# Performance work log

Measured on AMD Instinct MI355X. Metric: run time of the kernel, lower is better.

Reference implementation:

```python
import jax, jax.numpy as jnp
import numpy as np
import math

B, T, D, S, V = 128, 32, 64, 32, 8192
MAX_REC = 8
PONDER = 0.01
TWO_PI = 2.0 * math.pi


def setup_inputs():
    key = jax.random.key(0)
    ks = jax.random.split(key, 12)
    sd = 1.0 / math.sqrt(D)
    g = lambda k, shape, s: jax.random.normal(k, shape, jnp.float32) * s
    return {
        "x_seq": jax.random.randint(ks[0], (B, T), 0, V),
        "encoder_emb": g(ks[1], (V, 2 * D), 0.02),
        "vq_emb": g(ks[2], (V, 2 * D), sd),
        "norm_rg": jnp.ones((D,), jnp.float32), "norm_rb": jnp.zeros((D,), jnp.float32),
        "norm_ig": jnp.ones((D,), jnp.float32), "norm_ib": jnp.zeros((D,), jnp.float32),
        "qkv_Wr": g(ks[3], (3, D, D), sd), "qkv_br": g(ks[4], (3, D), sd),
        "qkv_Wi": g(ks[5], (3, D, D), sd), "qkv_bi": g(ks[6], (3, D), sd),
        "gate_w": g(ks[7], (2 * D,), sd), "gate_b": jnp.zeros((), jnp.float32),
        "arb_W": g(ks[8], (3, 2 * D), sd), "arb_b": jnp.zeros((3,), jnp.float32),
        "dec_W": g(ks[9], (V, 2 * D), sd), "dec_b": jnp.zeros((V,), jnp.float32),
        "halt_bias": jnp.asarray(3.0, jnp.float32),
        "input_gate": jnp.asarray(0.0, jnp.float32),
    }


def _ln(x, g, b, eps=1e-5):
    mu = x.mean(-1, keepdims=True)
    var = ((x - mu) ** 2).mean(-1, keepdims=True)
    return (x - mu) * jax.lax.rsqrt(var + eps) * g + b


def _forward(x_seq, encoder_emb, vq_emb, norm_rg, norm_rb, norm_ig, norm_ib,
             qkv_Wr, qkv_br, qkv_Wi, qkv_bi, gate_w, gate_b, arb_W, arb_b,
             dec_W, dec_b, halt_bias, input_gate):
    sg = jax.lax.stop_gradient
    e_sq = (vq_emb ** 2).sum(-1)  # [V]
    alpha = jax.nn.sigmoid(input_gate)
    bias = jax.nn.softplus(halt_bias)

    def clin(xr, xi, Wr, br, Wi, bi):
        # torch ComplexLinear: real = fc_r(xr) - fc_i(xi); imag = fc_r(xi) + fc_i(xr)
        return (xr @ Wr.T + br) - (xi @ Wi.T + bi), (xi @ Wr.T + br) + (xr @ Wi.T + bi)

    def mem_write(gr, gi, mr, mi):
        flat = jnp.concatenate([gr, gi], -1)
        wg = jax.nn.sigmoid(flat @ gate_w + gate_b)[:, None, None]  # [B,1,1]
        shr, shi = jnp.roll(mr, 1, axis=1), jnp.roll(mi, 1, axis=1)
        hr = wg * gr[:, None, :] + (1.0 - wg) * shr[:, :1]
        hi = wg * gi[:, None, :] + (1.0 - wg) * shi[:, :1]
        return jnp.concatenate([hr, shr[:, 1:]], 1), jnp.concatenate([hi, shi[:, 1:]], 1)

    def time_step(carry, xt):
        gw_r, gw_i, mem_r, mem_i = carry
        x_r, x_i = xt
        gw_r = alpha * gw_r + (1.0 - alpha) * x_r
        gw_i = alpha * gw_i + (1.0 - alpha) * x_i
        active = jnp.ones((B,), jnp.float32)
        acc_vq = jnp.zeros((B,), jnp.float32)
        acc_ent = jnp.zeros((B,), jnp.float32)
        acc_pond = jnp.zeros((B,), jnp.float32)
        acc_ph = jnp.zeros((B,), jnp.float32)
        fin_idx = jnp.zeros((B,), jnp.int32)
        prev_ang = jnp.arctan2(gw_i, gw_r)
        for _ in range(MAX_REC):
            cr = _ln(gw_r, norm_rg, norm_rb)
            ci = _ln(gw_i, norm_ig, norm_ib)
            z_flat = jnp.concatenate([cr, ci], -1)  # [B,2D]
            # squared-euclidean scores; argmin identical to cdist argmin
            d2 = (z_flat ** 2).sum(-1, keepdims=True) - 2.0 * (z_flat @ vq_emb.T) + e_sq
            idx = jnp.argmin(d2, -1).astype(jnp.int32)
            z_q = vq_emb[idx]
            vq_loss = ((z_q - sg(z_flat)) ** 2).mean(-1) + 0.25 * ((sg(z_q) - z_flat) ** 2).mean(-1)
            z_st = z_flat + sg(z_q - z_flat)  # straight-through
            counts = jnp.zeros((V,), jnp.float32).at[idx].add(1.0) / B
            entropy = -(counts * jnp.log(counts + 1e-10)).sum()
            v_r, v_i = z_st[:, :D], z_st[:, D:]
            # Hermitian gating
            qr, qi = clin(cr, ci, qkv_Wr[0], qkv_br[0], qkv_Wi[0], qkv_bi[0])
            kr, ki = clin(cr, ci, qkv_Wr[1], qkv_br[1], qkv_Wi[1], qkv_bi[1])
            vr2, vi2 = clin(cr, ci, qkv_Wr[2], qkv_br[2], qkv_Wi[2], qkv_bi[2])
            gate = jax.nn.sigmoid((qr * kr + qi * ki).sum(-1, keepdims=True))
            g_r, g_i = vr2 * gate, vi2 * gate
            # memory read (Re<m, q> attention over slots)
            sim = jnp.einsum('bsd,bd->bs', mem_r, cr) + jnp.einsum('bsd,bd->bs', mem_i, ci)
            attn = jax.nn.softmax(sim, -1)
            m_r = jnp.einsum('bs,bsd->bd', attn, mem_r)
            m_i = jnp.einsum('bs,bsd->bd', attn, mem_i)
            gates = jax.nn.softmax(z_flat @ arb_W.T + arb_b, -1)  # [B,3]
            upd_r = gates[:, 0:1] * g_r + gates[:, 1:2] * m_r + gates[:, 2:3] * v_r
            upd_i = gates[:, 0:1] * g_i + gates[:, 1:2] * m_i + gates[:, 2:3] * v_i
            cand_r = 0.6 * cr + 0.4 * upd_r
            cand_i = 0.6 * ci + 0.4 * upd_i
            ang = jnp.arctan2(cand_i, cand_r)
            diff = jnp.abs(ang - prev_ang)
            diff = jnp.minimum(diff, TWO_PI - diff)
            acc_ph = acc_ph + active * diff.mean(-1)
            prev_ang = ang
            halt_prob = jax.nn.sigmoid(bias - vq_loss)
            should_stop = (halt_prob > 0.5).astype(jnp.float32)
            acc_pond = acc_pond + active * PONDER
            mflat = active > 0.5
            acc_vq = jnp.where(mflat, vq_loss, acc_vq)
            acc_ent = jnp.where(mflat, entropy, acc_ent)
            fin_idx = jnp.where(mflat, idx, fin_idx)
            am = mflat[:, None]
            gw_r = jnp.where(am, cand_r, gw_r)
            gw_i = jnp.where(am, cand_i, gw_i)
            active = active * (1.0 - should_stop)
        mem_r, mem_i = mem_write(gw_r, gw_i, mem_r, mem_i)
        stats_t = jnp.stack([acc_vq.mean(), acc_ent.mean(), acc_pond.mean(), acc_ph.mean()])
        return (gw_r, gw_i, mem_r, mem_i), (gw_r, gw_i, fin_idx, stats_t)

    emb = encoder_emb[x_seq]  # [B,T,2D]
    xr = jnp.transpose(emb[..., :D], (1, 0, 2))  # [T,B,D]
    xi = jnp.transpose(emb[..., D:], (1, 0, 2))
    init = (jnp.zeros((B, D), jnp.float32), jnp.zeros((B, D), jnp.float32),
            jnp.zeros((B, S, D), jnp.float32), jnp.zeros((B, S, D), jnp.float32))
    _, (out_r, out_i, idxs, stats) = jax.lax.scan(time_step, init, (xr, xi))
    out = jnp.concatenate([jnp.transpose(out_r, (1, 0, 2)),
                           jnp.transpose(out_i, (1, 0, 2))], -1)  # [B,T,2D]
    logits = out @ dec_W.T + dec_b  # [B,T,V]
    return logits, stats.sum(0) / T, jnp.transpose(idxs)  # [B,T]


def reference(x_seq, encoder_emb, vq_emb, norm_rg, norm_rb, norm_ig, norm_ib, qkv_Wr, qkv_br, qkv_Wi, qkv_bi, gate_w, gate_b, arb_W, arb_b, dec_W, dec_b, halt_bias, input_gate):
    return _forward(x_seq, encoder_emb, vq_emb, norm_rg, norm_rb, norm_ig, norm_ib,
                    qkv_Wr, qkv_br, qkv_Wi, qkv_bi, gate_w, gate_b, arb_W, arb_b,
                    dec_W, dec_b, halt_bias, input_gate)
```

## Files before the change

kernel.cpp:

```cpp
#include <hip/hip_runtime.h>
#include <math.h>

#define TT 32
#define MAXREC 8
#define NBLK 256
#define NTHR 512

#define OFF_ZBUF   0u
#define OFF_ZBUFB  65536u
#define OFF_KEYS   98304u
#define OFF_ZDONE  229376u
#define OFF_ESQ    231424u
#define OFF_RST    264192u
#define OFF_OUTHB  266240u
#define OFF_WB     1314816u

#define SENT 0x7FFFFFFFu
#define IDXM 0x1FFFu
#define LOGN 33554432u
#define TWO_PI_F 6.283185307179586f

typedef float f32x4 __attribute__((ext_vector_type(4)));
typedef short bf16x8 __attribute__((ext_vector_type(8)));
typedef unsigned long long u64;

__device__ __forceinline__ float wredsum(float v) {
#pragma unroll
  for (int m = 32; m > 0; m >>= 1) v += __shfl_xor(v, m);
  return v;
}
__device__ __forceinline__ u64 shflx64(u64 v, int m) {
  int lo = __shfl_xor((int)(unsigned)(v & 0xffffffffull), m);
  int hi = __shfl_xor((int)(unsigned)(v >> 32), m);
  return ((u64)(unsigned)hi << 32) | (unsigned)lo;
}
__device__ __forceinline__ u64 packkey(float d, unsigned c) {
  unsigned u = __float_as_uint(d);
  u = (u & 0x80000000u) ? ~u : (u | 0x80000000u);
  return ((u64)u << 32) | c;
}
__device__ __forceinline__ float unpackd2(u64 key) {
  unsigned hi = (unsigned)(key >> 32);
  unsigned orig = (hi & 0x80000000u) ? (hi & 0x7fffffffu) : ~hi;
  return __uint_as_float(orig);
}
__device__ __forceinline__ unsigned short f2bf(float f) {
  unsigned u = __float_as_uint(f);
  unsigned r = (u >> 16) & 1u;
  u += 0x7fffu + r;
  return (unsigned short)(u >> 16);
}

__device__ __forceinline__ u64 ld_coh64(const u64* p) {
  u64 v;
  asm volatile("global_load_dwordx2 %0, %1, off sc0 sc1\n\ts_waitcnt vmcnt(0)"
               : "=&v"(v) : "v"(p) : "memory");
  return v;
}
__device__ __forceinline__ void st_coh_f32(float* p, float v) {
  asm volatile("global_store_dword %0, %1, off sc0 sc1" :: "v"(p), "v"(v) : "memory");
}
__device__ __forceinline__ void st_coh32(unsigned* p, unsigned v) {
  asm volatile("global_store_dword %0, %1, off sc0 sc1" :: "v"(p), "v"(v) : "memory");
}
__device__ __forceinline__ void st_coh64(u64* p, u64 v) {
  asm volatile("global_store_dwordx2 %0, %1, off sc0 sc1" :: "v"(p), "v"(v) : "memory");
}
__device__ __forceinline__ void drain_vm() {
  asm volatile("s_waitcnt vmcnt(0)" ::: "memory");
}
__device__ __forceinline__ void ld4w(const float* base,
    unsigned o0, unsigned o1, unsigned o2, unsigned o3,
    f32x4& a0, f32x4& a1, f32x4& a2, f32x4& a3) {
  asm volatile(
      "global_load_dwordx4 %0, %4, %8 sc0 sc1\n\t"
      "global_load_dwordx4 %1, %5, %8 sc0 sc1\n\t"
      "global_load_dwordx4 %2, %6, %8 sc0 sc1\n\t"
      "global_load_dwordx4 %3, %7, %8 sc0 sc1\n\t"
      "s_waitcnt vmcnt(0)"
      : "=&v"(a0), "=&v"(a1), "=&v"(a2), "=&v"(a3)
      : "v"(o0), "v"(o1), "v"(o2), "v"(o3), "s"(base)
      : "memory");
}

__global__ __launch_bounds__(512) void sacrsn_init(char* __restrict__ ws) {
  u64* zd = (u64*)(ws + OFF_ZDONE);
  u64* fin = (u64*)(ws + OFF_KEYS);
  (void)fin;
  if (threadIdx.x < 256) ((u64*)zd)[threadIdx.x] = 0ull;
}

__global__ __launch_bounds__(256) void k_prepv(const float* __restrict__ vqe,
                                               char* __restrict__ ws) {
  unsigned short* vqeB = (unsigned short*)(ws + OFF_WB);
  float* esqG = (float*)(ws + OFF_ESQ);
  const int i = (blockIdx.x * 256 + threadIdx.x) * 4;
  float4 v = *(const float4*)(vqe + i);
  ushort4 o;
  o.x = f2bf(v.x); o.y = f2bf(v.y); o.z = f2bf(v.z); o.w = f2bf(v.w);
  *(ushort4*)(vqeB + i) = o;
  if (blockIdx.x < 32) {
    const int c = blockIdx.x * 256 + threadIdx.x;
    const float4* e = (const float4*)(vqe + ((size_t)c << 7));
    float s = 0.f;
#pragma unroll 8
    for (int k4 = 0; k4 < 32; ++k4) {
      float4 q = e[k4];
      s = fmaf(q.x, q.x, fmaf(q.y, q.y, fmaf(q.z, q.z, fmaf(q.w, q.w, s))));
    }
    esqG[c] = s;
  }
}

__global__ __launch_bounds__(256) void k_prepd(const float* __restrict__ dW,
                                               char* __restrict__ ws) {
  unsigned short* dWb = (unsigned short*)(ws + OFF_WB);
  const int i = (blockIdx.x * 256 + threadIdx.x) * 4;
  float4 v = *(const float4*)(dW + i);
  ushort4 o;
  o.x = f2bf(v.x); o.y = f2bf(v.y); o.z = f2bf(v.z); o.w = f2bf(v.w);
  *(ushort4*)(dWb + i) = o;
}

__global__ __launch_bounds__(NTHR) void sacrsn_main(
    const int* __restrict__ x_seq, const float* __restrict__ enc,
    const float* __restrict__ vqe,
    const float* __restrict__ nrg, const float* __restrict__ nrb,
    const float* __restrict__ nig, const float* __restrict__ nib,
    const float* __restrict__ qWr, const float* __restrict__ qbr,
    const float* __restrict__ qWi, const float* __restrict__ qbi,
    const float* __restrict__ gtw, const float* __restrict__ gtb,
    const float* __restrict__ aW, const float* __restrict__ ab,
    const float* __restrict__ hbp, const float* __restrict__ igp,
    float* __restrict__ dout, char* __restrict__ ws)
{
  float* zbuf = (float*)(ws + OFF_ZBUF);
  unsigned* zbufB32 = (unsigned*)(ws + OFF_ZBUFB);
  u64*   keys = (u64*)(ws + OFF_KEYS);
  u64*   zdone64 = (u64*)(ws + OFF_ZDONE);
  const float* esqG = (const float*)(ws + OFF_ESQ);
  const unsigned short* vqeB = (const unsigned short*)(ws + OFF_WB);
  u64*   finalA = (u64*)(ws + OFF_KEYS);
  unsigned short* outhB = (unsigned short*)(ws + OFF_OUTHB);
  float* rst  = (float*)(ws + OFF_RST);
  finalA = (u64*)(ws + OFF_ZDONE + 1024u);
  finalA = (u64*)(ws + OFF_ZDONE + 8u);

  const int tid = threadIdx.x;
  const int wv = tid >> 6, ln = tid & 63;
  const int blk = blockIdx.x;
  const bool owner = (blk < 128);

  __shared__ float memLr[32 * 65];
  __shared__ float memLi[32 * 65];
  __shared__ float gwrowL[128], pangL[64], zfmL[128], zqL[128];
  __shared__ float qkL[6][64], simL[32], attnL[32], mrL[64], miL[64];
  __shared__ unsigned idxL[128] __attribute__((aligned(16)));
  __shared__ u64 key128L[128], kred[128];
  __shared__ float arbWL[3 * 128];
  __shared__ float scalL[8], entpL[2], vqpL[2], wsumL[2], z2pL[2];
  __shared__ float accL[4], totL[4];
  __shared__ float dmeanS;
  __shared__ u64 actM[2], actN[2];
  __shared__ unsigned pollOK, pollSent, mfS;
  __shared__ float z2L[128], sz2L[128];
  __shared__ u64 rowminU[128];
  __shared__ unsigned candL[8192];
  __shared__ unsigned candCount;

  const float alpha = 1.0f / (1.0f + expf(-igp[0]));
  const float onema = 1.0f - alpha;
  const float hbias = log1pf(expf(hbp[0]));
  const float gtb0 = gtb[0];

  if (!owner) {
    const int s = blk - 128;
    const int w = tid >> 6, l = tid & 63;
    const int ar = l & 15, kg = l >> 4;
    unsigned k = 0;
    while (true) {
      bool done = false;
      while (true) {
        if (tid == 0) { pollOK = 1u; pollSent = 1u; }
        __syncthreads();
        if (tid < 128) {
          u64 v = ld_coh64(&zdone64[tid * 2]);
          unsigned lo = (unsigned)v;
          if ((int)(lo - (k + 1u)) < 0) pollOK = 0u;
          if (lo != SENT) pollSent = 0u;
          if (lo == k + 1u) z2L[tid] = __uint_as_float((unsigned)(v >> 32));
        }
        __syncthreads();
        if (pollSent) { done = true; break; }
        if (pollOK) break;
        __builtin_amdgcn_s_sleep(1);
      }
      if (done) break;
      if (tid < 128) { sz2L[tid] = sqrtf(z2L[tid]); rowminU[tid] = ~0ull; }
      if (tid == 0) candCount = 0u;
      __syncthreads();
      f32x4 af0, af1, af2, af3;
      {
        const unsigned rb = (unsigned)((w * 16 + ar) * 256 + kg * 16);
        ld4w((const float*)(ws + OFF_ZBUFB), rb, rb + 64u, rb + 128u, rb + 192u,
             af0, af1, af2, af3);
      }
      bf16x8 afr[4];
      afr[0] = *(bf16x8*)&af0; afr[1] = *(bf16x8*)&af1;
      afr[2] = *(bf16x8*)&af2; afr[3] = *(bf16x8*)&af3;
      f32x4 dc[4];
#pragma unroll
      for (int nt = 0; nt < 4; ++nt) dc[nt] = (f32x4){0.f, 0.f, 0.f, 0.f};
#pragma unroll
      for (int kc = 0; kc < 4; ++kc) {
#pragma unroll
        for (int nt = 0; nt < 4; ++nt) {
          bf16x8 b = *(const bf16x8*)(vqeB + (((size_t)(s * 64 + nt * 16 + ar)) << 7)
                                      + kc * 32 + kg * 8);
          dc[nt] = __builtin_amdgcn_mfma_f32_16x16x32_bf16(afr[kc], b, dc[nt], 0, 0, 0);
        }
      }
      float aV[4][4], eV[4][4], Lmin[4];
#pragma unroll
      for (int rr = 0; rr < 4; ++rr) Lmin[rr] = 1e30f;
#pragma unroll
      for (int nt = 0; nt < 4; ++nt) {
        const int code = s * 64 + nt * 16 + ar;
        const float es = esqG[code];
        const float se = sqrtf(es);
#pragma unroll
        for (int rr = 0; rr < 4; ++rr) {
          const int row = w * 16 + kg * 4 + rr;
          float av = (z2L[row] - 2.0f * dc[nt][rr]) + es;
          float ev = fmaf(0.0082f * sz2L[row], se, 1e-3f);
          aV[nt][rr] = av; eV[nt][rr] = ev;
          float ae = av + ev;
          if (ae < Lmin[rr]) Lmin[rr] = ae;
        }
      }
#pragma unroll
      for (int m2 = 1; m2 < 16; m2 <<= 1)
#pragma unroll
        for (int rr = 0; rr < 4; ++rr) {
          float o = __shfl_xor(Lmin[rr], m2);
          if (o < Lmin[rr]) Lmin[rr] = o;
        }
#pragma unroll
      for (int nt = 0; nt < 4; ++nt)
#pragma unroll
        for (int rr = 0; rr < 4; ++rr)
          if (aV[nt][rr] - eV[nt][rr] <= Lmin[rr]) {
            const unsigned row = (unsigned)(w * 16 + kg * 4 + rr);
            const unsigned code = (unsigned)(s * 64 + nt * 16 + ar);
            unsigned pos = atomicAdd(&candCount, 1u);
            candL[pos] = (row << 16) | code;
          }
      __syncthreads();
      const unsigned cnt = candCount;
      for (unsigned base = 0; base < cnt; base += 64u) {
        const unsigned eIdx = base + (unsigned)(tid >> 3);
        const bool valid = eIdx < cnt;
        float dsum = 0.f;
        int row = 0, code = 0;
        if (valid) {
          unsigned en = candL[eIdx];
          row = (int)(en >> 16); code = (int)(en & 0xFFFFu);
          const int ks = tid & 7;
          f32x4 z0, z1, z2v, z3;
          const unsigned zb = (unsigned)(row * 512 + ks * 64);
          ld4w(zbuf, zb, zb + 16u, zb + 32u, zb + 48u, z0, z1, z2v, z3);
          const float4* ep = (const float4*)(vqe + ((size_t)code << 7) + ks * 16);
          float4 e0 = ep[0], e1 = ep[1], e2 = ep[2], e3 = ep[3];
          dsum = fmaf(z0[0], e0.x, fmaf(z0[1], e0.y, fmaf(z0[2], e0.z, fmaf(z0[3], e0.w, 0.f))));
          dsum = fmaf(z1[0], e1.x, fmaf(z1[1], e1.y, fmaf(z1[2], e1.z, fmaf(z1[3], e1.w, dsum))));
          dsum = fmaf(z2v[0], e2.x, fmaf(z2v[1], e2.y, fmaf(z2v[2], e2.z, fmaf(z2v[3], e2.w, dsum))));
          dsum = fmaf(z3[0], e3.x, fmaf(z3[1], e3.y, fmaf(z3[2], e3.z, fmaf(z3[3], e3.w, dsum))));
        }
#pragma unroll
        for (int m2 = 1; m2 < 8; m2 <<= 1) dsum += __shfl_xor(dsum, m2);
        if (valid && (tid & 7) == 0) {
          float d2 = (z2L[row] - 2.0f * dsum) + esqG[code];
          atomicMin(&rowminU[row], packkey(d2, (unsigned)code));
        }
      }
      __syncthreads();
      if (tid < 128)
        st_coh64(&keys[(size_t)s * 128 + tid], rowminU[tid] | ((u64)(k + 1u) << 13));
      k++;
    }
    return;
  }

  float lnG = 0.0f, lnB = 0.0f, gtwv = 0.0f;
  if (tid < 64) { lnG = nrg[tid]; lnB = nrb[tid]; }
  else if (tid < 128) { lnG = nig[tid - 64]; lnB = nib[tid - 64]; }
  if (tid < 128) gtwv = gtw[tid];
  for (int i = tid; i < 32 * 65; i += NTHR) { memLr[i] = 0.0f; memLi[i] = 0.0f; }
  if (tid < 4) { totL[tid] = 0.0f; accL[tid] = 0.0f; }
  if (tid < 2) actM[tid] = ~0ull;
  for (int i = tid; i < 384; i += NTHR) arbWL[i] = aW[i];
  {
    int tok = x_seq[blk * TT];
    if (tid < 128) gwrowL[tid] = onema * enc[((size_t)tok << 7) + tid];
  }
  __syncthreads();
  if (tid < 64) pangL[tid] = atan2f(gwrowL[64 + tid], gwrowL[tid]);
  if (tid < 128) {
    float val = gwrowL[tid];
    float mu = wredsum(val) * 0.015625f;
    float xc = val - mu;
    float vr = wredsum(xc * xc) * 0.015625f;
    float z = xc * (1.0f / sqrtf(vr + 1e-5f)) * lnG + lnB;
    zfmL[tid] = z;
    st_coh_f32(&zbuf[(blk << 7) + tid], z);
    float zo = __shfl_xor(z, 1);
    if ((tid & 1) == 0) {
      unsigned pk = (unsigned)f2bf(z) | ((unsigned)f2bf(zo) << 16);
      st_coh32(&zbufB32[blk * 64 + (tid >> 1)], pk);
    }
    float s2 = wredsum(z * z);
    if (ln == 0) z2pL[wv] = s2;
  }
  drain_vm();
  __syncthreads();
  if (tid == 0) {
    float z2 = z2pL[0] + z2pL[1];
    st_coh64(&zdone64[blk * 2], (u64)1u | ((u64)__float_as_uint(z2) << 32));
  }

  int t = 0, it = 0;
  unsigned k = 0;
  for (;;) {
    const unsigned tag = k + 1u;
    float encN = 0.0f;
    {
      int tnext = (t + 1 < TT) ? t + 1 : t;
      if (tid < 128) {
        int tk = x_seq[blk * TT + tnext];
        encN = enc[((size_t)tk << 7) + tid];
      }
    }
    if (tid < 192) {
      const int h = tid >> 6, j = tid & 63;
      const float* wr = qWr + h * 4096 + j * 64;
      const float* wi = qWi + h * 4096 + j * 64;
      float da = 0.0f, db_ = 0.0f, dc2 = 0.0f, de = 0.0f;
#pragma unroll 4
      for (int d4 = 0; d4 < 64; d4 += 4) {
        float4 wrv = *(const float4*)&wr[d4];
        float4 wiv = *(const float4*)&wi[d4];
        float4 crv = *(const float4*)&zfmL[d4];
        float4 civ = *(const float4*)&zfmL[64 + d4];
        da = fmaf(crv.x, wrv.x, fmaf(crv.y, wrv.y, fmaf(crv.z, wrv.z, fmaf(crv.w, wrv.w, da))));
        db_ = fmaf(civ.x, wiv.x, fmaf(civ.y, wiv.y, fmaf(civ.z, wiv.z, fmaf(civ.w, wiv.w, db_))));
        dc2 = fmaf(civ.x, wrv.x, fmaf(civ.y, wrv.y, fmaf(civ.z, wrv.z, fmaf(civ.w, wrv.w, dc2))));
        de = fmaf(crv.x, wiv.x, fmaf(crv.y, wiv.y, fmaf(crv.z, wiv.z, fmaf(crv.w, wiv.w, de))));
      }
      float brv = qbr[h * 64 + j], biv = qbi[h * 64 + j];
      qkL[2 * h][j] = da + brv - db_ - biv;
      qkL[2 * h + 1][j] = dc2 + brv + de + biv;
    } else if (tid < 224) {
      const int s2 = tid - 192;
      float a2 = 0.0f;
      for (int d = 0; d < 64; ++d)
        a2 = fmaf(memLr[s2 * 65 + d], zfmL[d], fmaf(memLi[s2 * 65 + d], zfmL[64 + d], a2));
      simL[s2] = a2;
    } else if (tid < 227) {
      const int h = tid - 224;
      float a2 = ab[h];
      for (int k2 = 0; k2 < 128; ++k2) a2 = fmaf(zfmL[k2], arbWL[h * 128 + k2], a2);
      scalL[3 + h] = a2;
    }
    __syncthreads();
    if (tid < 64) {
      float p = fmaf(qkL[0][tid], qkL[2][tid], qkL[1][tid] * qkL[3][tid]);
      p = wredsum(p);
      if (tid == 0) scalL[0] = 1.0f / (1.0f + expf(-p));
    } else if (tid < 96) {
      const int s2 = tid - 64;
      float v = simL[s2];
      float m = v;
#pragma unroll
      for (int msk = 16; msk > 0; msk >>= 1) m = fmaxf(m, __shfl_xor(m, msk));
      float e = expf(v - m);
      float ss = e;
#pragma unroll
      for (int msk = 16; msk > 0; msk >>= 1) ss += __shfl_xor(ss, msk);
      attnL[s2] = e / ss;
    } else if (tid == 96) {
      float a0 = scalL[3], a1 = scalL[4], a2 = scalL[5];
      float m = fmaxf(a0, fmaxf(a1, a2));
      float e0 = expf(a0 - m), e1 = expf(a1 - m), e2 = expf(a2 - m);
      float ssum = e0 + e1 + e2;
      scalL[3] = e0 / ssum; scalL[4] = e1 / ssum; scalL[5] = e2 / ssum;
    }
    __syncthreads();
    if (tid < 128) {
      const int d = ln;
      const float* ml = (wv == 0) ? memLr : memLi;
      float a2 = 0.0f;
#pragma unroll 4
      for (int s2 = 0; s2 < 32; ++s2) a2 = fmaf(attnL[s2], ml[s2 * 65 + d], a2);
      if (wv == 0) mrL[d] = a2; else miL[d] = a2;
    }
    while (true) {
      if (tid == 0) pollOK = 1u;
      __syncthreads();
      if (tid < 128) {
        u64 v = ld_coh64(&keys[(size_t)tid * 128 + blk]);
        if ((unsigned)((v >> 13) & 0x7FFFFull) != tag) pollOK = 0u;
        else kred[tid] = v;
      }
      __syncthreads();
      if (pollOK) break;
      __builtin_amdgcn_s_sleep(1);
    }
    if (tid < 64) {
      u64 a = kred[tid], b = kred[tid + 64];
      if (b < a) a = b;
#pragma unroll
      for (int m2 = 32; m2 > 0; m2 >>= 1) { u64 o = shflx64(a, m2); if (o < a) a = o; }
      if (tid == 0) st_coh64(&finalA[blk * 2], a);
    }
    while (true) {
      if (tid == 0) pollOK = 1u;
      __syncthreads();
      if (tid < 128) {
        u64 v = ld_coh64(&finalA[tid * 2]);
        if ((unsigned)((v >> 13) & 0x7FFFFull) != tag) pollOK = 0u;
        else key128L[tid] = v;
      }
      __syncthreads();
      if (pollOK) break;
      __builtin_amdgcn_s_sleep(1);
    }
    if (tid < 128) {
      u64 key = key128L[tid];
      idxL[tid] = (unsigned)key & IDXM;
      float d2 = unpackd2(key);
      bool act_b = ((actM[tid >> 6] >> (tid & 63)) & 1ull) != 0ull;
      bool stop = (1.25f * 0.0078125f * d2) < hbias;
      u64 ball = __ballot(act_b && !stop);
      if (ln == 0) actN[tid >> 6] = ball;
    }
    __syncthreads();
    if (tid == 0) mfS = (unsigned)((actM[blk >> 6] >> (blk & 63)) & 1ull);
    if (tid < 2) actM[tid] = actN[tid];
    __syncthreads();
    const bool anyAct = (actN[0] | actN[1]) != 0ull;
    const bool mf = mfS != 0u;
    const unsigned ii = idxL[blk];
    if (tid < 128) {
      float zq = vqe[((size_t)ii << 7) + tid];
      zqL[tid] = zq;
      float df = zq - zfmL[tid];
      float sm = wredsum(df * df);
      if (ln == 0) vqpL[wv] = sm;
    } else if (tid < 256) {
      const int r = tid - 128;
      unsigned my = idxL[r];
      int c = 0;
#pragma unroll
      for (int j4 = 0; j4 < 32; ++j4) {
        uint4 q = *(const uint4*)&idxL[j4 * 4];
        c += (q.x == my) + (q.y == my) + (q.z == my) + (q.w == my);
      }
      float term = -0.0078125f * logf((float)c * 0.0078125f + 1e-10f);
      term = wredsum(term);
      if (ln == 0) entpL[wv - 2] = term;
    }
    __syncthreads();
    if (tid < 64) {
      const int d = tid;
      float gate = scalL[0], g0 = scalL[3], g1 = scalL[4], g2 = scalL[5];
      float cr = zfmL[d], ci = zfmL[64 + d];
      float ur = fmaf(g0, qkL[4][d] * gate, fmaf(g1, mrL[d], g2 * zqL[d]));
      float ui = fmaf(g0, qkL[5][d] * gate, fmaf(g1, miL[d], g2 * zqL[64 + d]));
      float cdr = fmaf(0.4f, ur, 0.6f * cr);
      float cdi = fmaf(0.4f, ui, 0.6f * ci);
      float ang = atan2f(cdi, cdr);
      float df = fabsf(ang - pangL[d]);
      df = fminf(df, TWO_PI_F - df);
      pangL[d] = ang;
      float dm = wredsum(df) * 0.015625f;
      if (mf) { gwrowL[d] = cdr; gwrowL[64 + d] = cdi; }
      if (d == 0) dmeanS = dm;
    }
    __syncthreads();
    const bool newT = !(anyAct && it < MAXREC - 1);
    const bool finished = newT && (t == TT - 1);
    if (newT && !finished) {
      float pr = 0.0f;
      if (tid < 128) {
        pr = gwrowL[tid];
        outhB[((size_t)blk * TT + t) * 128 + tid] = f2bf(pr);
        float part = wredsum(pr * gtwv);
        if (ln == 0) wsumL[wv] = part;
      }
      __syncthreads();
      if (tid < 128) {
        float wg = 1.0f / (1.0f + expf(-(wsumL[0] + wsumL[1] + gtb0)));
        int slot = 31 - t;
        float* m = (tid < 64) ? &memLr[slot * 65 + tid] : &memLi[slot * 65 + (tid - 64)];
        *m = fmaf(wg, pr, (1.0f - wg) * (*m));
        gwrowL[tid] = fmaf(alpha, pr, onema * encN);
      }
      __syncthreads();
    }
    if (!finished) {
      if (tid < 128) {
        float val = gwrowL[tid];
        float mu = wredsum(val) * 0.015625f;
        float xc = val - mu;
        float vr = wredsum(xc * xc) * 0.015625f;
        float z = xc * (1.0f / sqrtf(vr + 1e-5f)) * lnG + lnB;
        zfmL[tid] = z;
        st_coh_f32(&zbuf[(blk << 7) + tid], z);
        float zo = __shfl_xor(z, 1);
        if ((tid & 1) == 0) {
          unsigned pk = (unsigned)f2bf(z) | ((unsigned)f2bf(zo) << 16);
          st_coh32(&zbufB32[blk * 64 + (tid >> 1)], pk);
        }
        float s2 = wredsum(z * z);
        if (ln == 0) z2pL[wv] = s2;
      }
      drain_vm();
      __syncthreads();
      if (tid == 0) {
        float z2 = z2pL[0] + z2pL[1];
        st_coh64(&zdone64[blk * 2], (u64)(k + 2u) | ((u64)__float_as_uint(z2) << 32));
      }
    } else {
      __syncthreads();
    }
    if (tid == 0) {
      float aold = mf ? 1.0f : 0.0f;
      float vql = 1.25f * (vqpL[0] + vqpL[1]) * 0.0078125f;
      accL[3] += aold * dmeanS;
      accL[2] += aold * 0.01f;
      if (mf) {
        accL[0] = vql;
        accL[1] = entpL[0] + entpL[1];
        dout[(size_t)LOGN + 4 + (size_t)blk * TT + t] = (float)ii;
      }
    }
    if (newT && !finished) {
      if (tid < 64) pangL[tid] = atan2f(gwrowL[64 + tid], gwrowL[tid]);
      if (tid < 4) { totL[tid] += accL[tid]; accL[tid] = 0.0f; }
      if (tid < 2) actM[tid] = ~0ull;
    }
    __syncthreads();
    if (finished) break;
    if (newT) { t++; it = 0; } else { it++; }
    k++;
  }

  if (tid < 128) outhB[((size_t)blk * TT + (TT - 1)) * 128 + tid] = f2bf(gwrowL[tid]);
  if (tid < 4) rst[blk * 4 + tid] = totL[tid] + accL[tid];
  __syncthreads();
  if (tid == 0) st_coh64(&zdone64[blk * 2], (u64)SENT);
}

__global__ __launch_bounds__(256) void k_dec(
    const float* __restrict__ dbv, float* __restrict__ dout,
    const char* __restrict__ ws)
{
  const unsigned short* outhB = (const unsigned short*)(ws + OFF_OUTHB);
  const unsigned short* dWb = (const unsigned short*)(ws + OFF_WB);
  const float* rst = (const float*)(ws + OFF_RST);
  const int tid = threadIdx.x;
  if (blockIdx.x == 0 && tid < 4) {
    float s = 0.0f;
    for (int r = 0; r < 128; ++r) s += rst[r * 4 + tid];
    dout[(size_t)LOGN + tid] = s * (1.0f / 4096.0f);
  }
  const int w = tid >> 6, l = tid & 63;
  const int bm = blockIdx.x & 63;
  const int bn = blockIdx.x >> 6;
  const int ar = l & 15, kg = l >> 4;
  const int m_base = bm * 64;
  const int n_base = bn * 256 + w * 64;
  f32x4 acc[4][4];
#pragma unroll
  for (int mt = 0; mt < 4; ++mt)
#pragma unroll
    for (int nt = 0; nt < 4; ++nt) acc[mt][nt] = (f32x4){0.f, 0.f, 0.f, 0.f};
#pragma unroll
  for (int kc = 0; kc < 4; ++kc) {
    const int ko = kc * 32 + kg * 8;
    bf16x8 a[4], b[4];
#pragma unroll
    for (int mt = 0; mt < 4; ++mt)
      a[mt] = *(const bf16x8*)(outhB + (size_t)(m_base + mt * 16 + ar) * 128 + ko);
#pragma unroll
    for (int nt = 0; nt < 4; ++nt)
      b[nt] = *(const bf16x8*)(dWb + (size_t)(n_base + nt * 16 + ar) * 128 + ko);
#pragma unroll
    for (int mt = 0; mt < 4; ++mt)
#pragma unroll
      for (int nt = 0; nt < 4; ++nt)
        acc[mt][nt] = __builtin_amdgcn_mfma_f32_16x16x32_bf16(a[mt], b[nt], acc[mt][nt], 0, 0, 0);
  }
#pragma unroll
  for (int nt = 0; nt < 4; ++nt) {
    const int n = n_base + nt * 16 + ar;
    const float bv = dbv[n];
#pragma unroll
    for (int mt = 0; mt < 4; ++mt) {
#pragma unroll
      for (int rr = 0; rr < 4; ++rr) {
        const int m = m_base + mt * 16 + kg * 4 + rr;
        dout[(size_t)m * 8192 + n] = acc[mt][nt][rr] + bv;
      }
    }
  }
}

extern "C" void kernel_launch(void* const* d_in, const int* in_sizes, int n_in,
                              void* d_out, int out_size, void* d_ws, size_t ws_size,
                              hipStream_t stream) {
  (void)in_sizes; (void)n_in; (void)out_size; (void)ws_size;
  const int*   x_seq = (const int*)d_in[0];
  const float* enc = (const float*)d_in[1];
  const float* vq  = (const float*)d_in[2];
  const float* nrg = (const float*)d_in[3];
  const float* nrb = (const float*)d_in[4];
  const float* nig = (const float*)d_in[5];
  const float* nib = (const float*)d_in[6];
  const float* qWr = (const float*)d_in[7];
  const float* qbr = (const float*)d_in[8];
  const float* qWi = (const float*)d_in[9];
  const float* qbi = (const float*)d_in[10];
  const float* gtw = (const float*)d_in[11];
  const float* gtb = (const float*)d_in[12];
  const float* aW  = (const float*)d_in[13];
  const float* ab  = (const float*)d_in[14];
  const float* dW  = (const float*)d_in[15];
  const float* db  = (const float*)d_in[16];
  const float* hb  = (const float*)d_in[17];
  const float* ig  = (const float*)d_in[18];
  char* ws = (char*)d_ws;
  float* out = (float*)d_out;
  hipLaunchKernelGGL(sacrsn_init, dim3(1), dim3(512), 0, stream, ws);
  hipLaunchKernelGGL(k_prepv, dim3(1024), dim3(256), 0, stream, vq, ws);
  hipLaunchKernelGGL(sacrsn_main, dim3(NBLK), dim3(NTHR), 0, stream,
                     x_seq, enc, vq, nrg, nrb, nig, nib, qWr, qbr, qWi, qbi,
                     gtw, gtb, aW, ab, hb, ig, out, ws);
  hipLaunchKernelGGL(k_prepd, dim3(1024), dim3(256), 0, stream, dW, ws);
  hipLaunchKernelGGL(k_dec, dim3(2048), dim3(256), 0, stream, db, out, ws);
}
```

Measured before the change: 698.0 us.

## Replace block-wide polling with per-wave ballot polling and defer off-critical-path stats

Replaces the shared-flag polling loops, which needed two __syncthreads per spin, with per-wave loads and __all/__any votes, so each wave waits on its own rows only. Codebook worker blocks reset their row minima and candidate count right after publishing, which removes a barrier per step. The owner blocks now do the codebook lookup for the chosen code alongside the halting ballot, and the phase-angle and entropy statistics move after the state is published so they no longer sit on the cross-block critical path. The candidate refinement uses 4 lanes per candidate instead of 8. The risk is subtle ordering bugs in the cross-block handshake and extra shared-memory reuse of mrL/miL as scratch.

After: 721.4 us. +3.3%, slower.

```diff
diff --git a/kernel.cpp b/kernel.cpp
--- a/kernel.cpp
+++ b/kernel.cpp
@@ -82,12 +82,32 @@
       : "v"(o0), "v"(o1), "v"(o2), "v"(o3), "s"(base)
       : "memory");
 }
+__device__ __forceinline__ void ld8w(const float* base,
+    unsigned o0, unsigned o1, unsigned o2, unsigned o3,
+    unsigned o4, unsigned o5, unsigned o6, unsigned o7,
+    f32x4& a0, f32x4& a1, f32x4& a2, f32x4& a3,
+    f32x4& a4, f32x4& a5, f32x4& a6, f32x4& a7) {
+  asm volatile(
+      "global_load_dwordx4 %0, %8, %16 sc0 sc1\n\t"
+      "global_load_dwordx4 %1, %9, %16 sc0 sc1\n\t"
+      "global_load_dwordx4 %2, %10, %16 sc0 sc1\n\t"
+      "global_load_dwordx4 %3, %11, %16 sc0 sc1\n\t"
+      "global_load_dwordx4 %4, %12, %16 sc0 sc1\n\t"
+      "global_load_dwordx4 %5, %13, %16 sc0 sc1\n\t"
+      "global_load_dwordx4 %6, %14, %16 sc0 sc1\n\t"
+      "global_load_dwordx4 %7, %15, %16 sc0 sc1\n\t"
+      "s_waitcnt vmcnt(0)"
+      : "=&v"(a0), "=&v"(a1), "=&v"(a2), "=&v"(a3),
+        "=&v"(a4), "=&v"(a5), "=&v"(a6), "=&v"(a7)
+      : "v"(o0), "v"(o1), "v"(o2), "v"(o3),
+        "v"(o4), "v"(o5), "v"(o6), "v"(o7),
+        "s"(base)
+      : "memory");
+}
 
 __global__ __launch_bounds__(512) void sacrsn_init(char* __restrict__ ws) {
   u64* zd = (u64*)(ws + OFF_ZDONE);
-  u64* fin = (u64*)(ws + OFF_KEYS);
-  (void)fin;
-  if (threadIdx.x < 256) ((u64*)zd)[threadIdx.x] = 0ull;
+  if (threadIdx.x < 256) zd[threadIdx.x] = 0ull;
 }
 
 __global__ __launch_bounds__(256) void k_prepv(const float* __restrict__ vqe,
@@ -138,13 +158,11 @@
   unsigned* zbufB32 = (unsigned*)(ws + OFF_ZBUFB);
   u64*   keys = (u64*)(ws + OFF_KEYS);
   u64*   zdone64 = (u64*)(ws + OFF_ZDONE);
+  u64*   finalA = (u64*)(ws + OFF_ZDONE + 8u);
   const float* esqG = (const float*)(ws + OFF_ESQ);
   const unsigned short* vqeB = (const unsigned short*)(ws + OFF_WB);
-  u64*   finalA = (u64*)(ws + OFF_KEYS);
   unsigned short* outhB = (unsigned short*)(ws + OFF_OUTHB);
   float* rst  = (float*)(ws + OFF_RST);
-  finalA = (u64*)(ws + OFF_ZDONE + 1024u);
-  finalA = (u64*)(ws + OFF_ZDONE + 8u);
 
   const int tid = threadIdx.x;
   const int wv = tid >> 6, ln = tid & 63;
@@ -162,7 +180,6 @@
   __shared__ float accL[4], totL[4];
   __shared__ float dmeanS;
   __shared__ u64 actM[2], actN[2];
-  __shared__ unsigned pollOK, pollSent, mfS;
   __shared__ float z2L[128], sz2L[128];
   __shared__ u64 rowminU[128];
   __shared__ unsigned candL[8192];
@@ -177,31 +194,36 @@
     const int s = blk - 128;
     const int w = tid >> 6, l = tid & 63;
     const int ar = l & 15, kg = l >> 4;
+    const int rowbase = w * 16;
+    if (tid < 128) rowminU[tid] = ~0ull;
+    if (tid == 0) candCount = 0u;
+    __syncthreads();
     unsigned k = 0;
     while (true) {
-      bool done = false;
-      while (true) {
-        if (tid == 0) { pollOK = 1u; pollSent = 1u; }
-        __syncthreads();
-        if (tid < 128) {
-          u64 v = ld_coh64(&zdone64[tid * 2]);
-          unsigned lo = (unsigned)v;
-          if ((int)(lo - (k + 1u)) < 0) pollOK = 0u;
-          if (lo != SENT) pollSent = 0u;
-          if (lo == k + 1u) z2L[tid] = __uint_as_float((unsigned)(v >> 32));
+      u64 tv;
+      bool done;
+      {
+        const u64* tp = &zdone64[(size_t)(rowbase + ar) * 2];
+        bool sent;
+        while (true) {
+          tv = ld_coh64(tp);
+          unsigned lo = (unsigned)tv;
+          sent = (lo == SENT);
+          bool ok = (lo == k + 1u) || sent;
+          if (__all(ok)) break;
+          __builtin_amdgcn_s_sleep(1);
         }
-        __syncthreads();
-        if (pollSent) { done = true; break; }
-        if (pollOK) break;
-        __builtin_amdgcn_s_sleep(1);
+        done = __any(sent);
       }
       if (done) break;
-      if (tid < 128) { sz2L[tid] = sqrtf(z2L[tid]); rowminU[tid] = ~0ull; }
-      if (tid == 0) candCount = 0u;
-      __syncthreads();
+      {
+        float z2 = __uint_as_float((unsigned)(tv >> 32));
+        z2L[rowbase + ar] = z2;
+        sz2L[rowbase + ar] = sqrtf(z2);
+      }
       f32x4 af0, af1, af2, af3;
       {
-        const unsigned rb = (unsigned)((w * 16 + ar) * 256 + kg * 16);
+        const unsigned rb = (unsigned)((rowbase + ar) * 256 + kg * 16);
         ld4w((const float*)(ws + OFF_ZBUFB), rb, rb + 64u, rb + 128u, rb + 192u,
              af0, af1, af2, af3);
       }
@@ -230,7 +252,7 @@
         const float se = sqrtf(es);
 #pragma unroll
         for (int rr = 0; rr < 4; ++rr) {
-          const int row = w * 16 + kg * 4 + rr;
+          const int row = rowbase + kg * 4 + rr;
           float av = (z2L[row] - 2.0f * dc[nt][rr]) + es;
           float ev = fmaf(0.0082f * sz2L[row], se, 1e-3f);
           aV[nt][rr] = av; eV[nt][rr] = ev;
@@ -250,42 +272,53 @@
 #pragma unroll
         for (int rr = 0; rr < 4; ++rr)
           if (aV[nt][rr] - eV[nt][rr] <= Lmin[rr]) {
-            const unsigned row = (unsigned)(w * 16 + kg * 4 + rr);
+            const unsigned row = (unsigned)(rowbase + kg * 4 + rr);
             const unsigned code = (unsigned)(s * 64 + nt * 16 + ar);
             unsigned pos = atomicAdd(&candCount, 1u);
             candL[pos] = (row << 16) | code;
           }
       __syncthreads();
       const unsigned cnt = candCount;
-      for (unsigned base = 0; base < cnt; base += 64u) {
-        const unsigned eIdx = base + (unsigned)(tid >> 3);
-        const bool valid = eIdx < cnt;
+      for (unsigned base = 0; base < cnt; base += 128u) {
+        const unsigned eI = base + (unsigned)(tid >> 2);
+        const int sub = tid & 3;
+        const bool valid = eI < cnt;
         float dsum = 0.f;
         int row = 0, code = 0;
         if (valid) {
-          unsigned en = candL[eIdx];
+          unsigned en = candL[eI];
           row = (int)(en >> 16); code = (int)(en & 0xFFFFu);
-          const int ks = tid & 7;
-          f32x4 z0, z1, z2v, z3;
-          const unsigned zb = (unsigned)(row * 512 + ks * 64);
-          ld4w(zbuf, zb, zb + 16u, zb + 32u, zb + 48u, z0, z1, z2v, z3);
-          const float4* ep = (const float4*)(vqe + ((size_t)code << 7) + ks * 16);
+          f32x4 zv0, zv1, zv2, zv3, zv4, zv5, zv6, zv7;
+          const unsigned zb = (unsigned)(row * 512 + sub * 128);
+          ld8w(zbuf, zb, zb + 16u, zb + 32u, zb + 48u,
+               zb + 64u, zb + 80u, zb + 96u, zb + 112u,
+               zv0, zv1, zv2, zv3, zv4, zv5, zv6, zv7);
+          const float4* ep = (const float4*)(vqe + ((size_t)code << 7) + sub * 32);
           float4 e0 = ep[0], e1 = ep[1], e2 = ep[2], e3 = ep[3];
-          dsum = fmaf(z0[0], e0.x, fmaf(z0[1], e0.y, fmaf(z0[2], e0.z, fmaf(z0[3], e0.w, 0.f))));
-          dsum = fmaf(z1[0], e1.x, fmaf(z1[1], e1.y, fmaf(z1[2], e1.z, fmaf(z1[3], e1.w, dsum))));
-          dsum = fmaf(z2v[0], e2.x, fmaf(z2v[1], e2.y, fmaf(z2v[2], e2.z, fmaf(z2v[3], e2.w, dsum))));
-          dsum = fmaf(z3[0], e3.x, fmaf(z3[1], e3.y, fmaf(z3[2], e3.z, fmaf(z3[3], e3.w, dsum))));
+          float4 e4 = ep[4], e5 = ep[5], e6 = ep[6], e7 = ep[7];
+          dsum = fmaf(zv0[0], e0.x, fmaf(zv0[1], e0.y, fmaf(zv0[2], e0.z, fmaf(zv0[3], e0.w, 0.f))));
+          dsum = fmaf(zv1[0], e1.x, fmaf(zv1[1], e1.y, fmaf(zv1[2], e1.z, fmaf(zv1[3], e1.w, dsum))));
+          dsum = fmaf(zv2[0], e2.x, fmaf(zv2[1], e2.y, fmaf(zv2[2], e2.z, fmaf(zv2[3], e2.w, dsum))));
+          dsum = fmaf(zv3[0], e3.x, fmaf(zv3[1], e3.y, fmaf(zv3[2], e3.z, fmaf(zv3[3], e3.w, dsum))));
+          dsum = fmaf(zv4[0], e4.x, fmaf(zv4[1], e4.y, fmaf(zv4[2], e4.z, fmaf(zv4[3], e4.w, dsum))));
+          dsum = fmaf(zv5[0], e5.x, fmaf(zv5[1], e5.y, fmaf(zv5[2], e5.z, fmaf(zv5[3], e5.w, dsum))));
+          dsum = fmaf(zv6[0], e6.x, fmaf(zv6[1], e6.y, fmaf(zv6[2], e6.z, fmaf(zv6[3], e6.w, dsum))));
+          dsum = fmaf(zv7[0], e7.x, fmaf(zv7[1], e7.y, fmaf(zv7[2], e7.z, fmaf(zv7[3], e7.w, dsum))));
         }
-#pragma unroll
-        for (int m2 = 1; m2 < 8; m2 <<= 1) dsum += __shfl_xor(dsum, m2);
-        if (valid && (tid & 7) == 0) {
+        dsum += __shfl_xor(dsum, 1);
+        dsum += __shfl_xor(dsum, 2);
+        if (valid && sub == 0) {
           float d2 = (z2L[row] - 2.0f * dsum) + esqG[code];
           atomicMin(&rowminU[row], packkey(d2, (unsigned)code));
         }
       }
       __syncthreads();
-      if (tid < 128)
-        st_coh64(&keys[(size_t)s * 128 + tid], rowminU[tid] | ((u64)(k + 1u) << 13));
+      if (tid < 128) {
+        u64 kk = rowminU[tid];
+        rowminU[tid] = ~0ull;
+        if (tid == 0) candCount = 0u;
+        st_coh64(&keys[(size_t)s * 128 + tid], kk | ((u64)(k + 1u) << 13));
+      }
       k++;
     }
     return;
@@ -403,18 +436,17 @@
       for (int s2 = 0; s2 < 32; ++s2) a2 = fmaf(attnL[s2], ml[s2 * 65 + d], a2);
       if (wv == 0) mrL[d] = a2; else miL[d] = a2;
     }
-    while (true) {
-      if (tid == 0) pollOK = 1u;
-      __syncthreads();
-      if (tid < 128) {
-        u64 v = ld_coh64(&keys[(size_t)tid * 128 + blk]);
-        if ((unsigned)((v >> 13) & 0x7FFFFull) != tag) pollOK = 0u;
-        else kred[tid] = v;
-      }
-      __syncthreads();
-      if (pollOK) break;
-      __builtin_amdgcn_s_sleep(1);
-    }
+    if (tid < 128) {
+      const u64* kp = &keys[(size_t)tid * 128 + blk];
+      u64 v;
+      while (true) {
+        v = ld_coh64(kp);
+        if (__all(((unsigned)(v >> 13) & 0x7FFFFu) == tag)) break;
+        __builtin_amdgcn_s_sleep(1);
+      }
+      kred[tid] = v;
+    }
+    __syncthreads();
     if (tid < 64) {
       u64 a = kred[tid], b = kred[tid + 64];
       if (b < a) a = b;
@@ -422,18 +454,18 @@
       for (int m2 = 32; m2 > 0; m2 >>= 1) { u64 o = shflx64(a, m2); if (o < a) a = o; }
       if (tid == 0) st_coh64(&finalA[blk * 2], a);
     }
-    while (true) {
-      if (tid == 0) pollOK = 1u;
-      __syncthreads();
-      if (tid < 128) {
-        u64 v = ld_coh64(&finalA[tid * 2]);
-        if ((unsigned)((v >> 13) & 0x7FFFFull) != tag) pollOK = 0u;
-        else key128L[tid] = v;
-      }
-      __syncthreads();
-      if (pollOK) break;
-      __builtin_amdgcn_s_sleep(1);
-    }
+    if (tid < 128) {
+      const u64* fp = &finalA[(size_t)tid * 2];
+      u64 v;
+      while (true) {
+        v = ld_coh64(fp);
+        if (__all(((unsigned)(v >> 13) & 0x7FFFFu) == tag)) break;
+        __builtin_amdgcn_s_sleep(1);
+      }
+      key128L[tid] = v;
+    }
+    __syncthreads();
+    const bool aoldb = ((actM[blk >> 6] >> (blk & 63)) & 1ull) != 0ull;
     if (tid < 128) {
       u64 key = key128L[tid];
       idxL[tid] = (unsigned)key & IDXM;
@@ -442,34 +474,19 @@
       bool stop = (1.25f * 0.0078125f * d2) < hbias;
       u64 ball = __ballot(act_b && !stop);
       if (ln == 0) actN[tid >> 6] = ball;
-    }
-    __syncthreads();
-    if (tid == 0) mfS = (unsigned)((actM[blk >> 6] >> (blk & 63)) & 1ull);
+    } else if (tid < 256) {
+      const int d = tid - 128;
+      unsigned ii2 = (unsigned)key128L[blk] & IDXM;
+      float zq = vqe[((size_t)ii2 << 7) + d];
+      zqL[d] = zq;
+      float df = zq - zfmL[d];
+      float sm = wredsum(df * df);
+      if (ln == 0) vqpL[wv - 2] = sm;
+    }
+    __syncthreads();
+    const bool anyAct = (actN[0] | actN[1]) != 0ull;
+    const bool mf = aoldb;
     if (tid < 2) actM[tid] = actN[tid];
-    __syncthreads();
-    const bool anyAct = (actN[0] | actN[1]) != 0ull;
-    const bool mf = mfS != 0u;
-    const unsigned ii = idxL[blk];
-    if (tid < 128) {
-      float zq = vqe[((size_t)ii << 7) + tid];
-      zqL[tid] = zq;
-      float df = zq - zfmL[tid];
-      float sm = wredsum(df * df);
-      if (ln == 0) vqpL[wv] = sm;
-    } else if (tid < 256) {
-      const int r = tid - 128;
-      unsigned my = idxL[r];
-      int c = 0;
-#pragma unroll
-      for (int j4 = 0; j4 < 32; ++j4) {
-        uint4 q = *(const uint4*)&idxL[j4 * 4];
-        c += (q.x == my) + (q.y == my) + (q.z == my) + (q.w == my);
-      }
-      float term = -0.0078125f * logf((float)c * 0.0078125f + 1e-10f);
-      term = wredsum(term);
-      if (ln == 0) entpL[wv - 2] = term;
-    }
-    __syncthreads();
     if (tid < 64) {
       const int d = tid;
       float gate = scalL[0], g0 = scalL[3], g1 = scalL[4], g2 = scalL[5];
@@ -478,13 +495,8 @@
       float ui = fmaf(g0, qkL[5][d] * gate, fmaf(g1, miL[d], g2 * zqL[64 + d]));
       float cdr = fmaf(0.4f, ur, 0.6f * cr);
       float cdi = fmaf(0.4f, ui, 0.6f * ci);
-      float ang = atan2f(cdi, cdr);
-      float df = fabsf(ang - pangL[d]);
-      df = fminf(df, TWO_PI_F - df);
-      pangL[d] = ang;
-      float dm = wredsum(df) * 0.015625f;
+      mrL[d] = cdr; miL[d] = cdi;
       if (mf) { gwrowL[d] = cdr; gwrowL[64 + d] = cdi; }
-      if (d == 0) dmeanS = dm;
     }
     __syncthreads();
     const bool newT = !(anyAct && it < MAXREC - 1);
@@ -533,6 +545,29 @@
     } else {
       __syncthreads();
     }
+    if (tid < 64) {
+      const int d = tid;
+      float cdr = mrL[d], cdi = miL[d];
+      float ang = atan2f(cdi, cdr);
+      float df = fabsf(ang - pangL[d]);
+      df = fminf(df, TWO_PI_F - df);
+      pangL[d] = ang;
+      float dm = wredsum(df) * 0.015625f;
+      if (d == 0) dmeanS = dm;
+    } else if (tid >= 128 && tid < 256) {
+      const int r = tid - 128;
+      unsigned my = idxL[r];
+      int c = 0;
+#pragma unroll
+      for (int j4 = 0; j4 < 32; ++j4) {
+        uint4 q = *(const uint4*)&idxL[j4 * 4];
+        c += (q.x == my) + (q.y == my) + (q.z == my) + (q.w == my);
+      }
+      float term = -0.0078125f * logf((float)c * 0.0078125f + 1e-10f);
+      term = wredsum(term);
+      if (ln == 0) entpL[wv - 2] = term;
+    }
+    __syncthreads();
     if (tid == 0) {
       float aold = mf ? 1.0f : 0.0f;
       float vql = 1.25f * (vqpL[0] + vqpL[1]) * 0.0078125f;
@@ -541,7 +576,7 @@
       if (mf) {
         accL[0] = vql;
         accL[1] = entpL[0] + entpL[1];
-        dout[(size_t)LOGN + 4 + (size_t)blk * TT + t] = (float)ii;
+        dout[(size_t)LOGN + 4 + (size_t)blk * TT + t] = (float)idxL[blk];
       }
     }
     if (newT && !finished) {
```
